# Performance work log

Hardware: AMD Instinct MI355X
Metric: run time of the kernel (lower is better)

The kernel has to match this reference:

```python
import jax, jax.numpy as jnp
import numpy as np

S = 2048   # sample_batch
N = 16     # num_h (agents per sample group)
OBS = 8
PRED = 12
H = 16     # hidden / embed size


def _lstm_cell(x, h, c, Wi, Wh, b):
    # torch LSTMCell gate order: i, f, g, o
    g = x @ Wi + h @ Wh + b
    i, f, gg, o = jnp.split(g, 4, axis=-1)
    c = jax.nn.sigmoid(f) * c + jax.nn.sigmoid(i) * jnp.tanh(gg)
    h = jax.nn.sigmoid(o) * jnp.tanh(c)
    return h, c


def setup_inputs() -> dict:
    key = jax.random.key(0)
    ks = jax.random.split(key, 16)
    B = S * N
    p = lambda k, sh: jax.random.normal(k, sh, jnp.float32) * 0.1
    return dict(
        traj_rel=jax.random.normal(ks[0], (OBS, B, 2), jnp.float32),
        obs_traj_pos=jax.random.normal(ks[1], (OBS, B, 2), jnp.float32),
        nei_index=jax.random.randint(ks[2], (B, N), 0, 2, jnp.int32),
        noise=jax.random.normal(ks[3], (PRED, B, 2), jnp.float32),
        enc_emb_W=p(ks[4], (2, H)), enc_emb_b=jnp.zeros((H,), jnp.float32),
        enc_Wi=p(ks[5], (H, 4 * H)), enc_Wh=p(ks[6], (H, 4 * H)), enc_b=jnp.zeros((4 * H,), jnp.float32),
        dec_in_W=p(ks[7], (H + 2, H)), dec_in_b=jnp.zeros((H,), jnp.float32),
        dec_Wi=p(ks[8], (H, 4 * H)), dec_Wh=p(ks[9], (H, 4 * H)), dec_b=jnp.zeros((4 * H,), jnp.float32),
        pool_rel_W=p(ks[10], (2, H)), pool_rel_b=jnp.zeros((H,), jnp.float32),
        pool_mlp_W=p(ks[11], (2 * H, H)), pool_mlp_b=jnp.zeros((H,), jnp.float32),
        out_W=p(ks[12], (H, 4)), out_b=jnp.zeros((4,), jnp.float32),
    )


def reference(traj_rel, obs_traj_pos, nei_index, noise,
              enc_emb_W, enc_emb_b, enc_Wi, enc_Wh, enc_b,
              dec_in_W, dec_in_b, dec_Wi, dec_Wh, dec_b,
              pool_rel_W, pool_rel_b, pool_mlp_W, pool_mlp_b,
              out_W, out_b):
    B = traj_rel.shape[1]
    mask = nei_index > 0  # (B, N)

    # --- history encoder: embed + LSTM over obs steps, take last hidden ---
    def enc_step(carry, x):
        h, c = carry
        e = jax.nn.relu(x @ enc_emb_W + enc_emb_b)
        h, c = _lstm_cell(e, h, c, enc_Wi, enc_Wh, enc_b)
        return (h, c), None

    h0 = jnp.zeros((B, H), traj_rel.dtype)
    (h_enc, _), _ = jax.lax.scan(enc_step, (h0, h0), traj_rel[:OBS])

    # --- neighbor pooling: embed relative pos, concat neighbor hidden, MLP, masked max-pool ---
    def pool(rel, h):
        re = jax.nn.relu(rel @ pool_rel_W + pool_rel_b)  # (B, N, H)
        hn = jnp.broadcast_to(h.reshape(S, 1, N, H), (S, N, N, H)).reshape(B, N, H)
        feat = jax.nn.relu(jnp.concatenate([re, hn], -1) @ pool_mlp_W + pool_mlp_b)
        masked = jnp.where(mask[..., None], feat, -1e9)
        pooled = masked.max(axis=1)  # (B, H)
        has = mask.any(axis=1, keepdims=True)
        return jnp.where(has, pooled, 0.0)

    def dec_step(carry, noise_t):
        h, c, ctx, out, pos = carry
        inp = jax.lax.stop_gradient(jnp.concatenate([ctx, out], -1))  # .detach() in torch
        e = jax.nn.relu(inp @ dec_in_W + dec_in_b)
        h, c = _lstm_cell(e, h, c, dec_Wi, dec_Wh, dec_b)
        p = pos.reshape(S, N, 2)
        # rel[s,i,j] = pos[s,i] - pos[s,j]  (matches expand/transpose subtraction)
        rel = (p[:, :, None, :] - p[:, None, :, :]).reshape(B, N, 2)
        ctx = pool(rel, h)
        o4 = (h + ctx) @ out_W + out_b
        mu = o4[:, :2]
        scale = jnp.clip(o4[:, 2:], -9.0, 4.0)
        std = jnp.exp(scale)
        pred = mu + std * noise_t
        pos = jax.lax.stop_gradient(pos + pred)
        return (h, c, ctx, pred, pos), (pred, mu, std)

    init = (h_enc, jnp.zeros_like(h_enc), jnp.zeros_like(h_enc),
            traj_rel[OBS - 1], obs_traj_pos[-1])
    _, (pred, mu, std) = jax.lax.scan(dec_step, init, noise)
    return pred, mu, std  # each (PRED, B, 2)
```

## Files before the change

### kernel.cpp

```cpp
#include <hip/hip_runtime.h>

#define S_    2048
#define N_    16
#define OBS_  8
#define PRED_ 12
#define B_    (S_*N_)
#define SCN_  2

typedef __attribute__((ext_vector_type(8))) short short8;
typedef __attribute__((ext_vector_type(4))) float floatx4;
typedef __attribute__((ext_vector_type(2))) float floatx2;
typedef __attribute__((ext_vector_type(4))) unsigned uintx4;
typedef unsigned short ushort_t;

#if __has_builtin(__builtin_elementwise_fma) && __has_builtin(__builtin_elementwise_max)
#define HAVE_PK 1
#define FMA2(a,b,c) __builtin_elementwise_fma((a),(b),(c))
#define MAX2(a,b)   __builtin_elementwise_max((a),(b))
#else
#define HAVE_PK 0
#endif

__device__ __forceinline__ float sigmf(float x) { return __builtin_amdgcn_rcpf(1.0f + __expf(-x)); }
__device__ __forceinline__ float tanhx(float x) { return fmaf(-2.0f, __builtin_amdgcn_rcpf(1.0f + __expf(2.0f*x)), 1.0f); }
__device__ __forceinline__ unsigned bfhi(float f) {
  return __builtin_bit_cast(unsigned, f) + 0x8000u;
}
__device__ __forceinline__ unsigned pack2bf(float lo, float hi) {
  return __builtin_amdgcn_perm(bfhi(hi), bfhi(lo), 0x07060302);
}
__device__ __forceinline__ ushort_t f2bf1(float f) { return (ushort_t)(bfhi(f) >> 16); }
__device__ __forceinline__ float rlanef(float v, int lane) {
  return __builtin_bit_cast(float, __builtin_amdgcn_readlane(__builtin_bit_cast(int, v), lane));
}
__device__ __forceinline__ unsigned shflu(unsigned v, int src) {
  return (unsigned)__shfl((int)v, src, 64);
}
__device__ __forceinline__ unsigned shflxu(unsigned v, int m) {
  return (unsigned)__shfl_xor((int)v, m, 64);
}

extern "C" __global__ __launch_bounds__(128, 2) void traj_ar_kernel(
    const float* __restrict__ traj_rel, const float* __restrict__ obs_pos,
    const int*  __restrict__ nei,       const float* __restrict__ noise,
    const float* __restrict__ eeW, const float* __restrict__ eeb,
    const float* __restrict__ eWi, const float* __restrict__ eWh, const float* __restrict__ eb,
    const float* __restrict__ diW, const float* __restrict__ dib,
    const float* __restrict__ dWi, const float* __restrict__ dWh, const float* __restrict__ db,
    const float* __restrict__ prW, const float* __restrict__ prb,
    const float* __restrict__ mW,  const float* __restrict__ mb,
    const float* __restrict__ oW,  const float* __restrict__ ob,
    float* __restrict__ out)
{
  __shared__ __align__(16) ushort_t ctx_bf[SCN_][384];
  __shared__            unsigned sm_s[SCN_][16];

  const int tid = threadIdx.x;
  const int w  = tid >> 6;
  const int l  = tid & 63;
  const int lq = l >> 4;
  const int lc = l & 15;
  const int u0 = lq*4;
  const int s  = blockIdx.x*SCN_ + w;
  const bool hi_half = (lq >= 2);
  const int esrc0 = (lq & 1)*32 + lc;
  const int esrc1 = esrc0 + 16;

  {
    unsigned* cz = (unsigned*)ctx_bf[w];
    cz[l] = 0; cz[64+l] = 0; cz[128+l] = 0;
  }
  float POSX = obs_pos[((OBS_-1)*B_ + s*N_ + lc)*2 + 0];
  float POSY = obs_pos[((OBS_-1)*B_ + s*N_ + lc)*2 + 1];
  unsigned prevu;
  {
    float pvx = traj_rel[((OBS_-1)*B_ + s*N_ + lc)*2 + 0];
    float pvy = traj_rel[((OBS_-1)*B_ + s*N_ + lc)*2 + 1];
    prevu = pack2bf(pvx, pvy);
  }
  {
    const int a = l >> 2, nb = (l & 3)*4;
    const int4 nv = *(const int4*)&nei[(s*N_ + a)*N_ + nb];
    unsigned bits = 0;
    bits |= (nv.x > 0) ? (1u << (nb+0)) : 0u;
    bits |= (nv.y > 0) ? (1u << (nb+1)) : 0u;
    bits |= (nv.z > 0) ? (1u << (nb+2)) : 0u;
    bits |= (nv.w > 0) ? (1u << (nb+3)) : 0u;
    bits |= __shfl_xor(bits, 1, 64);
    bits |= __shfl_xor(bits, 2, 64);
    if ((l & 3) == 0) sm_s[w][a] = bits;
  }

  short8 bfrag;
  {
    uintx4 bw;
    #pragma unroll
    for (int p = 0; p < 4; ++p)
      bw[p] = pack2bf(mW[(8*lq + 2*p)*16 + lc], mW[(8*lq + 2*p + 1)*16 + lc]);
    bfrag = __builtin_bit_cast(short8, bw);
  }
  const float bm = mb[lc];

#if HAVE_PK
  floatx2 pWx2[4], pWy2[4], pB2[4];
  {
    const int wu0 = (lq & 1) * 8;
    #pragma unroll
    for (int jj = 0; jj < 4; ++jj) {
      pWx2[jj] = (floatx2){prW[wu0 + 2*jj],      prW[wu0 + 2*jj + 1]};
      pWy2[jj] = (floatx2){prW[16 + wu0 + 2*jj], prW[16 + wu0 + 2*jj + 1]};
      pB2[jj]  = (floatx2){prb[wu0 + 2*jj],      prb[wu0 + 2*jj + 1]};
    }
  }
#else
  float pWx[8], pWy[8], pB[8];
  {
    const int wu0 = (lq & 1) * 8;
    #pragma unroll
    for (int j = 0; j < 8; ++j) {
      pWx[j] = prW[wu0 + j];
      pWy[j] = prW[16 + wu0 + j];
      pB[j]  = prb[wu0 + j];
    }
  }
#endif

  short8 oA; floatx4 oC;
  {
    uintx4 aw; aw[0]=0; aw[1]=0; aw[2]=0; aw[3]=0;
    if (lc < 4) {
      #pragma unroll
      for (int p = 0; p < 4; ++p)
        aw[p] = pack2bf(oW[((lq&1)*8 + 2*p)*4 + lc], oW[((lq&1)*8 + 2*p + 1)*4 + lc]);
    }
    oA = __builtin_bit_cast(short8, aw);
    #pragma unroll
    for (int r = 0; r < 4; ++r) oC[r] = (lq == 0) ? ob[r] : 0.0f;
  }

  float ew0[4], ew1[4], ebv[4];
  #pragma unroll
  for (int r = 0; r < 4; ++r) {
    ew0[r] = eeW[u0+r]; ew1[r] = eeW[16+u0+r]; ebv[r] = eeb[u0+r];
  }

  const int row0 = (lq & 1) * 8;

  #define LOAD_GATE_FRAG(A, C, Wi_, Wh_, bias_, g) {                                      \
    const float* gsrc_ = (lq & 2) ? (Wh_) : (Wi_);                                        \
    uintx4 aw_;                                                                           \
    aw_[0] = pack2bf(gsrc_[(row0+0)*64 + (g)*16 + lc], gsrc_[(row0+1)*64 + (g)*16 + lc]); \
    aw_[1] = pack2bf(gsrc_[(row0+2)*64 + (g)*16 + lc], gsrc_[(row0+3)*64 + (g)*16 + lc]); \
    aw_[2] = pack2bf(gsrc_[(row0+4)*64 + (g)*16 + lc], gsrc_[(row0+5)*64 + (g)*16 + lc]); \
    aw_[3] = pack2bf(gsrc_[(row0+6)*64 + (g)*16 + lc], gsrc_[(row0+7)*64 + (g)*16 + lc]); \
    (A) = __builtin_bit_cast(short8, aw_);                                                \
    (C)[0] = (bias_)[(g)*16 + u0 + 0]; (C)[1] = (bias_)[(g)*16 + u0 + 1];                 \
    (C)[2] = (bias_)[(g)*16 + u0 + 2]; (C)[3] = (bias_)[(g)*16 + u0 + 3];                 \
  }

  short8 eA0, eA1, eA2, eA3; floatx4 eC0, eC1, eC2, eC3;
  LOAD_GATE_FRAG(eA0, eC0, eWi, eWh, eb, 0);
  LOAD_GATE_FRAG(eA1, eC1, eWi, eWh, eb, 1);
  LOAD_GATE_FRAG(eA2, eC2, eWi, eWh, eb, 2);
  LOAD_GATE_FRAG(eA3, eC3, eWi, eWh, eb, 3);

  #define LSTM_EW(r, hv) {                                                            \
    float ig = sigmf(dI[r]), fg = sigmf(dF[r]), gv = tanhx(dG[r]), og = sigmf(dO[r]); \
    c4[r] = fg*c4[r] + ig*gv;                                                         \
    hv = og * tanhx(c4[r]);                                                           \
  }

  uintx4 hf; hf[0]=0; hf[1]=0; hf[2]=0; hf[3]=0;

  floatx4 c4 = {0.0f, 0.0f, 0.0f, 0.0f};
  const float2* xr2 = (const float2*)traj_rel;
  for (int t = 0; t < OBS_; ++t) {
    float2 x = xr2[t*B_ + s*N_ + lc];
    float e0 = fmaxf(fmaf(x.y, ew1[0], fmaf(x.x, ew0[0], ebv[0])), 0.0f);
    float e1 = fmaxf(fmaf(x.y, ew1[1], fmaf(x.x, ew0[1], ebv[1])), 0.0f);
    float e2 = fmaxf(fmaf(x.y, ew1[2], fmaf(x.x, ew0[2], ebv[2])), 0.0f);
    float e3 = fmaxf(fmaf(x.y, ew1[3], fmaf(x.x, ew0[3], ebv[3])), 0.0f);
    uint2 ep; ep.x = pack2bf(e0, e1); ep.y = pack2bf(e2, e3);
    uintx4 eu;
    eu[0] = shflu(ep.x, esrc0); eu[1] = shflu(ep.y, esrc0);
    eu[2] = shflu(ep.x, esrc1); eu[3] = shflu(ep.y, esrc1);
    uintx4 bu = (lq < 2) ? eu : hf;
    short8 bfr = __builtin_bit_cast(short8, bu);
    floatx4 dI = __builtin_amdgcn_mfma_f32_16x16x32_bf16(eA0, bfr, eC0, 0, 0, 0);
    floatx4 dF = __builtin_amdgcn_mfma_f32_16x16x32_bf16(eA1, bfr, eC1, 0, 0, 0);
    floatx4 dG = __builtin_amdgcn_mfma_f32_16x16x32_bf16(eA2, bfr, eC2, 0, 0, 0);
    floatx4 dO = __builtin_amdgcn_mfma_f32_16x16x32_bf16(eA3, bfr, eC3, 0, 0, 0);
    float h40, h41, h42, h43;
    LSTM_EW(0, h40); LSTM_EW(1, h41); LSTM_EW(2, h42); LSTM_EW(3, h43);
    uint2 hp2; hp2.x = pack2bf(h40, h41); hp2.y = pack2bf(h42, h43);
    hf[0] = shflu(hp2.x, esrc0); hf[1] = shflu(hp2.y, esrc0);
    hf[2] = shflu(hp2.x, esrc1); hf[3] = shflu(hp2.y, esrc1);
  }

  short8 dA0, dA1, dA2, dA3; floatx4 dC0, dC1, dC2, dC3;
  LOAD_GATE_FRAG(dA0, dC0, dWi, dWh, db, 0);
  LOAD_GATE_FRAG(dA1, dC1, dWi, dWh, db, 1);
  LOAD_GATE_FRAG(dA2, dC2, dWi, dWh, db, 2);
  LOAD_GATE_FRAG(dA3, dC3, dWi, dWh, db, 3);

  short8 diA; floatx4 diC;
  {
    uintx4 aw; aw[0]=0; aw[1]=0; aw[2]=0; aw[3]=0;
    if (lq < 2) {
      const int r0 = lq*8;
      #pragma unroll
      for (int p = 0; p < 4; ++p)
        aw[p] = pack2bf(diW[(r0+2*p)*16 + lc], diW[(r0+2*p+1)*16 + lc]);
    } else if (lq == 2) {
      aw[0] = pack2bf(diW[16*16 + lc], diW[17*16 + lc]);
    }
    diA = __builtin_bit_cast(short8, aw);
    #pragma unroll
    for (int r = 0; r < 4; ++r) diC[r] = dib[u0 + r];
  }

  floatx4 cm[16];
  #pragma unroll
  for (int tt = 0; tt < 16; ++tt) {
    const unsigned mi = sm_s[w][tt];
    #pragma unroll
    for (int r = 0; r < 4; ++r)
      cm[tt][r] = ((mi >> (u0 + r)) & 1u) ? bm : -1e9f;
  }

  #define MK_REFRAG(pp, F0, F1) {                                           \
    const int t0_ = 2*(pp), t1_ = 2*(pp)+1;                                 \
    float rx0_ = PXs[t0_] - POSX, ry0_ = PYs[t0_] - POSY;                   \
    float rx1_ = PXs[t1_] - POSX, ry1_ = PYs[t1_] - POSY;                   \
    float rx_ = hi_half ? rx1_ : rx0_;                                      \
    float ry_ = hi_half ? ry1_ : ry0_;                                      \
    MK_RR_BODY(F0)                                                          \
    (F1)[0] = shflxu((F0)[0], 32);                                          \
    (F1)[1] = shflxu((F0)[1], 32);                                          \
    (F1)[2] = shflxu((F0)[2], 32);                                          \
    (F1)[3] = shflxu((F0)[3], 32);                                          \
  }

#if HAVE_PK
  #define MK_RR_BODY(F0) {                                                  \
    const floatx2 rx2_ = {rx_, rx_}, ry2_ = {ry_, ry_};                     \
    const floatx2 z2_ = {0.0f, 0.0f};                                       \
    floatx2 q0_ = MAX2(FMA2(ry2_, pWy2[0], FMA2(rx2_, pWx2[0], pB2[0])), z2_); \
    floatx2 q1_ = MAX2(FMA2(ry2_, pWy2[1], FMA2(rx2_, pWx2[1], pB2[1])), z2_); \
    floatx2 q2_ = MAX2(FMA2(ry2_, pWy2[2], FMA2(rx2_, pWx2[2], pB2[2])), z2_); \
    floatx2 q3_ = MAX2(FMA2(ry2_, pWy2[3], FMA2(rx2_, pWx2[3], pB2[3])), z2_); \
    (F0)[0] = pack2bf(q0_.x, q0_.y);                                        \
    (F0)[1] = pack2bf(q1_.x, q1_.y);                                        \
    (F0)[2] = pack2bf(q2_.x, q2_.y);                                        \
    (F0)[3] = pack2bf(q3_.x, q3_.y);                                        \
  }
#else
  #define MK_RR_BODY(F0) {                                                  \
    float rr_[8];                                                           \
    _Pragma("unroll")                                                       \
    for (int j = 0; j < 8; ++j)                                             \
      rr_[j] = fmaxf(fmaf(ry_, pWy[j], fmaf(rx_, pWx[j], pB[j])), 0.0f);    \
    (F0)[0] = pack2bf(rr_[0], rr_[1]);                                      \
    (F0)[1] = pack2bf(rr_[2], rr_[3]);                                      \
    (F0)[2] = pack2bf(rr_[4], rr_[5]);                                      \
    (F0)[3] = pack2bf(rr_[6], rr_[7]);                                      \
  }
#endif

  #define POOL_TILE(tt, FRAG) {                                             \
    short8 a_ = hi_half ? __builtin_bit_cast(short8, hf)                    \
                        : __builtin_bit_cast(short8, FRAG);                 \
    floatx4 d_ = __builtin_amdgcn_mfma_f32_16x16x32_bf16(a_, bfrag, cm[tt], 0, 0, 0); \
    float pm_ = fmaxf(fmaxf(fmaxf(d_[0], d_[1]), d_[2]), d_[3]);            \
    pm_ = fmaxf(pm_, __shfl_xor(pm_, 16, 64));                              \
    pm_ = fmaxf(pm_, __shfl_xor(pm_, 32, 64));                              \
    if (lq == ((tt) & 3)) {                                                 \
      ctx_bf[w][(tt)*24 + lc] = f2bf1(fmaxf(pm_, 0.0f));                    \
    }                                                                       \
  }

  c4 = (floatx4){0.0f, 0.0f, 0.0f, 0.0f};
  const int MU_OFF = PRED_*B_*2;
  const int SD_OFF = 2*PRED_*B_*2;
  const float2* nz2p = (const float2*)noise;
  short8 cvN = *(const short8*)&ctx_bf[w][lc*24 + (lq&1)*8];
  for (int t = 0; t < PRED_; ++t) {
    const float2 nz2 = nz2p[t*B_ + s*N_ + lc];
    float PXs[16], PYs[16];
    #pragma unroll
    for (int a2 = 0; a2 < 16; ++a2) {
      PXs[a2] = rlanef(POSX, a2);
      PYs[a2] = rlanef(POSY, a2);
    }
    uintx4 g0, g1;
    MK_REFRAG(0, g0, g1);
    uint2 ep;
    {
      uintx4 pz; pz[0] = prevu; pz[1]=0; pz[2]=0; pz[3]=0;
      short8 pv = __builtin_bit_cast(short8, pz);
      short8 zz = {0,0,0,0,0,0,0,0};
      short8 bf1 = (lq < 2) ? cvN : ((lq == 2) ? pv : zz);
      __builtin_amdgcn_s_setprio(1);
      floatx4 d = __builtin_amdgcn_mfma_f32_16x16x32_bf16(diA, bf1, diC, 0, 0, 0);
      __builtin_amdgcn_s_setprio(0);
      ep.x = pack2bf(fmaxf(d[0],0.0f), fmaxf(d[1],0.0f));
      ep.y = pack2bf(fmaxf(d[2],0.0f), fmaxf(d[3],0.0f));
    }
    {
      uintx4 eu;
      eu[0] = shflu(ep.x, esrc0); eu[1] = shflu(ep.y, esrc0);
      eu[2] = shflu(ep.x, esrc1); eu[3] = shflu(ep.y, esrc1);
      uintx4 bu = (lq < 2) ? eu : hf;
      short8 bfr = __builtin_bit_cast(short8, bu);
      __builtin_amdgcn_s_setprio(1);
      floatx4 dI = __builtin_amdgcn_mfma_f32_16x16x32_bf16(dA0, bfr, dC0, 0, 0, 0);
      floatx4 dF = __builtin_amdgcn_mfma_f32_16x16x32_bf16(dA1, bfr, dC1, 0, 0, 0);
      floatx4 dG = __builtin_amdgcn_mfma_f32_16x16x32_bf16(dA2, bfr, dC2, 0, 0, 0);
      floatx4 dO = __builtin_amdgcn_mfma_f32_16x16x32_bf16(dA3, bfr, dC3, 0, 0, 0);
      __builtin_amdgcn_s_setprio(0);
      float h40, h41, h42, h43;
      LSTM_EW(0, h40); LSTM_EW(1, h41); LSTM_EW(2, h42); LSTM_EW(3, h43);
      uint2 hp2; hp2.x = pack2bf(h40, h41); hp2.y = pack2bf(h42, h43);
      hf[0] = shflu(hp2.x, esrc0); hf[1] = shflu(hp2.y, esrc0);
      hf[2] = shflu(hp2.x, esrc1); hf[3] = shflu(hp2.y, esrc1);
    }
    {
      #pragma unroll
      for (int p = 0; p < 8; ++p) {
        uintx4 n0, n1;
        if (p < 7) MK_REFRAG(p+1, n0, n1);
        POOL_TILE(2*p,     g0);
        POOL_TILE(2*p + 1, g1);
        g0 = n0; g1 = n1;
      }
    }
    cvN = *(const short8*)&ctx_bf[w][lc*24 + (lq&1)*8];
    {
      uintx4 bu = (lq < 2) ? __builtin_bit_cast(uintx4, cvN) : hf;
      short8 bfr = __builtin_bit_cast(short8, bu);
      floatx4 d = __builtin_amdgcn_mfma_f32_16x16x32_bf16(oA, bfr, oC, 0, 0, 0);
      float mux = d[0], muy = d[1];
      float scx = fminf(fmaxf(d[2], -9.0f), 4.0f);
      float scy = fminf(fmaxf(d[3], -9.0f), 4.0f);
      float sdx = __expf(scx);
      float sdy = __expf(scy);
      float prxv = fmaf(sdx, nz2.x, mux);
      float pryv = fmaf(sdy, nz2.y, muy);
      if (lq == 0) {
        int o = (t*B_ + s*N_ + lc)*2;
        float2 v0; v0.x = prxv; v0.y = pryv;
        float2 v1; v1.x = mux;  v1.y = muy;
        float2 v2; v2.x = sdx;  v2.y = sdy;
        *(float2*)&out[o]          = v0;
        *(float2*)&out[MU_OFF + o] = v1;
        *(float2*)&out[SD_OFF + o] = v2;
      }
      float prx = __shfl(prxv, lc, 64);
      float pry = __shfl(pryv, lc, 64);
      POSX += prx;
      POSY += pry;
      prevu = pack2bf(prx, pry);
    }
  }
  #undef LSTM_EW
  #undef LOAD_GATE_FRAG
  #undef MK_REFRAG
  #undef MK_RR_BODY
  #undef POOL_TILE
}

extern "C" void kernel_launch(void* const* d_in, const int* in_sizes, int n_in,
                              void* d_out, int out_size, void* d_ws, size_t ws_size,
                              hipStream_t stream) {
  (void)in_sizes; (void)n_in; (void)d_ws; (void)ws_size; (void)out_size;
  traj_ar_kernel<<<dim3(S_/SCN_), dim3(128), 0, stream>>>(
      (const float*)d_in[0],  (const float*)d_in[1],  (const int*)d_in[2],   (const float*)d_in[3],
      (const float*)d_in[4],  (const float*)d_in[5],  (const float*)d_in[6], (const float*)d_in[7],
      (const float*)d_in[8],  (const float*)d_in[9],  (const float*)d_in[10],(const float*)d_in[11],
      (const float*)d_in[12], (const float*)d_in[13], (const float*)d_in[14],(const float*)d_in[15],
      (const float*)d_in[16], (const float*)d_in[17], (const float*)d_in[18],(const float*)d_in[19],
      (float*)d_out);
}
```

Measured before the change: 155.8 us.

## Split each sample's pooling across two wavefronts with double-buffered shared context

Each block now handles one sample with two wavefronts instead of two samples with one wavefront each. The two waves share the 16 pooling tiles, eight each, and exchange results through a double-buffered shared ctx array with one barrier per step. The LSTM and output work is duplicated in both waves, and only wave 0 writes results. The aim is to halve the serial pooling chain per wave and raise occupancy through launch bounds of 4. The cost is redundant LSTM work and a block barrier in every timestep.

Result: slower. 180.2 us (+15.7%).

```diff
diff --git a/kernel.cpp b/kernel.cpp
--- a/kernel.cpp
+++ b/kernel.cpp
@@ -5,7 +5,6 @@
 #define OBS_  8
 #define PRED_ 12
 #define B_    (S_*N_)
-#define SCN_  2
 
 typedef __attribute__((ext_vector_type(8))) short short8;
 typedef __attribute__((ext_vector_type(4))) float floatx4;
@@ -40,7 +39,7 @@
   return (unsigned)__shfl_xor((int)v, m, 64);
 }
 
-extern "C" __global__ __launch_bounds__(128, 2) void traj_ar_kernel(
+extern "C" __global__ __launch_bounds__(128, 4) void traj_ar_kernel(
     const float* __restrict__ traj_rel, const float* __restrict__ obs_pos,
     const int*  __restrict__ nei,       const float* __restrict__ noise,
     const float* __restrict__ eeW, const float* __restrict__ eeb,
@@ -52,23 +51,23 @@
     const float* __restrict__ oW,  const float* __restrict__ ob,
     float* __restrict__ out)
 {
-  __shared__ __align__(16) ushort_t ctx_bf[SCN_][384];
-  __shared__            unsigned sm_s[SCN_][16];
+  __shared__ __align__(16) ushort_t ctx_bf[2][384];
+  __shared__            unsigned sm_s[16];
 
   const int tid = threadIdx.x;
-  const int w  = tid >> 6;
   const int l  = tid & 63;
   const int lq = l >> 4;
   const int lc = l & 15;
   const int u0 = lq*4;
-  const int s  = blockIdx.x*SCN_ + w;
+  const int wvi = __builtin_amdgcn_readfirstlane(tid >> 6);
+  const int s  = blockIdx.x;
   const bool hi_half = (lq >= 2);
   const int esrc0 = (lq & 1)*32 + lc;
   const int esrc1 = esrc0 + 16;
 
   {
-    unsigned* cz = (unsigned*)ctx_bf[w];
-    cz[l] = 0; cz[64+l] = 0; cz[128+l] = 0;
+    unsigned* cz = (unsigned*)ctx_bf;
+    cz[tid] = 0; cz[128+tid] = 0; cz[256+tid] = 0;
   }
   float POSX = obs_pos[((OBS_-1)*B_ + s*N_ + lc)*2 + 0];
   float POSY = obs_pos[((OBS_-1)*B_ + s*N_ + lc)*2 + 1];
@@ -88,8 +87,9 @@
     bits |= (nv.w > 0) ? (1u << (nb+3)) : 0u;
     bits |= __shfl_xor(bits, 1, 64);
     bits |= __shfl_xor(bits, 2, 64);
-    if ((l & 3) == 0) sm_s[w][a] = bits;
-  }
+    if ((l & 3) == 0) sm_s[a] = bits;
+  }
+  __syncthreads();
 
   short8 bfrag;
   {
@@ -219,19 +219,19 @@
     for (int r = 0; r < 4; ++r) diC[r] = dib[u0 + r];
   }
 
-  floatx4 cm[16];
+  floatx4 cm[8];
   #pragma unroll
-  for (int tt = 0; tt < 16; ++tt) {
-    const unsigned mi = sm_s[w][tt];
+  for (int k = 0; k < 8; ++k) {
+    const unsigned mi = sm_s[wvi*8 + k];
     #pragma unroll
     for (int r = 0; r < 4; ++r)
-      cm[tt][r] = ((mi >> (u0 + r)) & 1u) ? bm : -1e9f;
+      cm[k][r] = ((mi >> (u0 + r)) & 1u) ? bm : -1e9f;
   }
 
   #define MK_REFRAG(pp, F0, F1) {                                           \
-    const int t0_ = 2*(pp), t1_ = 2*(pp)+1;                                 \
-    float rx0_ = PXs[t0_] - POSX, ry0_ = PYs[t0_] - POSY;                   \
-    float rx1_ = PXs[t1_] - POSX, ry1_ = PYs[t1_] - POSY;                   \
+    const int t0_ = wvi*8 + 2*(pp), t1_ = t0_ + 1;                          \
+    float rx0_ = rlanef(POSX, t0_) - POSX, ry0_ = rlanef(POSY, t0_) - POSY; \
+    float rx1_ = rlanef(POSX, t1_) - POSX, ry1_ = rlanef(POSY, t1_) - POSY; \
     float rx_ = hi_half ? rx1_ : rx0_;                                      \
     float ry_ = hi_half ? ry1_ : ry0_;                                      \
     MK_RR_BODY(F0)                                                          \
@@ -267,15 +267,15 @@
   }
 #endif
 
-  #define POOL_TILE(tt, FRAG) {                                             \
+  #define POOL_TILE(k, FRAG) {                                              \
     short8 a_ = hi_half ? __builtin_bit_cast(short8, hf)                    \
                         : __builtin_bit_cast(short8, FRAG);                 \
-    floatx4 d_ = __builtin_amdgcn_mfma_f32_16x16x32_bf16(a_, bfrag, cm[tt], 0, 0, 0); \
+    floatx4 d_ = __builtin_amdgcn_mfma_f32_16x16x32_bf16(a_, bfrag, cm[k], 0, 0, 0); \
     float pm_ = fmaxf(fmaxf(fmaxf(d_[0], d_[1]), d_[2]), d_[3]);            \
     pm_ = fmaxf(pm_, __shfl_xor(pm_, 16, 64));                              \
     pm_ = fmaxf(pm_, __shfl_xor(pm_, 32, 64));                              \
-    if (lq == ((tt) & 3)) {                                                 \
-      ctx_bf[w][(tt)*24 + lc] = f2bf1(fmaxf(pm_, 0.0f));                    \
+    if (lq == ((k) & 3)) {                                                  \
+      cbW[(wvi*8 + (k))*24 + lc] = f2bf1(fmaxf(pm_, 0.0f));                 \
     }                                                                       \
   }
 
@@ -283,15 +283,10 @@
   const int MU_OFF = PRED_*B_*2;
   const int SD_OFF = 2*PRED_*B_*2;
   const float2* nz2p = (const float2*)noise;
-  short8 cvN = *(const short8*)&ctx_bf[w][lc*24 + (lq&1)*8];
+  short8 cvN = *(const short8*)&ctx_bf[1][lc*24 + (lq&1)*8];
   for (int t = 0; t < PRED_; ++t) {
+    ushort_t* cbW = ctx_bf[t & 1];
     const float2 nz2 = nz2p[t*B_ + s*N_ + lc];
-    float PXs[16], PYs[16];
-    #pragma unroll
-    for (int a2 = 0; a2 < 16; ++a2) {
-      PXs[a2] = rlanef(POSX, a2);
-      PYs[a2] = rlanef(POSY, a2);
-    }
     uintx4 g0, g1;
     MK_REFRAG(0, g0, g1);
     uint2 ep;
@@ -326,15 +321,16 @@
     }
     {
       #pragma unroll
-      for (int p = 0; p < 8; ++p) {
+      for (int p = 0; p < 4; ++p) {
         uintx4 n0, n1;
-        if (p < 7) MK_REFRAG(p+1, n0, n1);
+        if (p < 3) MK_REFRAG(p+1, n0, n1);
         POOL_TILE(2*p,     g0);
         POOL_TILE(2*p + 1, g1);
         g0 = n0; g1 = n1;
       }
     }
-    cvN = *(const short8*)&ctx_bf[w][lc*24 + (lq&1)*8];
+    __syncthreads();
+    cvN = *(const short8*)&cbW[lc*24 + (lq&1)*8];
     {
       uintx4 bu = (lq < 2) ? __builtin_bit_cast(uintx4, cvN) : hf;
       short8 bfr = __builtin_bit_cast(short8, bu);
@@ -346,7 +342,7 @@
       float sdy = __expf(scy);
       float prxv = fmaf(sdx, nz2.x, mux);
       float pryv = fmaf(sdy, nz2.y, muy);
-      if (lq == 0) {
+      if (wvi == 0 && lq == 0) {
         int o = (t*B_ + s*N_ + lc)*2;
         float2 v0; v0.x = prxv; v0.y = pryv;
         float2 v1; v1.x = mux;  v1.y = muy;
@@ -373,7 +369,7 @@
                               void* d_out, int out_size, void* d_ws, size_t ws_size,
                               hipStream_t stream) {
   (void)in_sizes; (void)n_in; (void)d_ws; (void)ws_size; (void)out_size;
-  traj_ar_kernel<<<dim3(S_/SCN_), dim3(128), 0, stream>>>(
+  traj_ar_kernel<<<dim3(S_), dim3(128), 0, stream>>>(
       (const float*)d_in[0],  (const float*)d_in[1],  (const int*)d_in[2],   (const float*)d_in[3],
       (const float*)d_in[4],  (const float*)d_in[5],  (const float*)d_in[6], (const float*)d_in[7],
       (const float*)d_in[8],  (const float*)d_in[9],  (const float*)d_in[10],(const float*)d_in[11],
```
